# Performance work log

Measured on AMD Instinct MI355X. Metric: run time of the kernel, lower is better.

The kernel has to match this reference:

```python
import jax, jax.numpy as jnp
import numpy as np
import math

B, N, DHID, NH, DHEAD, DFF = 2, 1024, 512, 16, 32, 2048
FACTOR = 0.5 / math.sqrt(DHEAD)


def _ln(x, g, b):
    m = jnp.mean(x, -1, keepdims=True)
    v = jnp.mean((x - m) ** 2, -1, keepdims=True)
    return (x - m) / jnp.sqrt(v + 1e-5) * g + b


def setup_inputs() -> dict:
    key = jax.random.key(0)
    ks = jax.random.split(key, 16)
    rn = lambda k, s, sc=0.02: jax.random.normal(k, s, jnp.float32) * sc
    inp = {}
    inp["H"] = jax.random.normal(ks[0], (B, N, DHID), jnp.float32)
    inp["V"] = jax.random.normal(ks[1], (B, N, 3, DHID), jnp.float32)
    inp["D"] = jax.random.normal(ks[2], (B, N, N), jnp.float32)
    inp["rbf"] = jax.random.normal(ks[3], (B, NH, N, N), jnp.float32)
    inp["mask"] = jnp.ones((B, N), jnp.int32)
    # attention params
    inp["Wq"] = rn(ks[4], (DHID, 4 * DHID)); inp["bq"] = jnp.zeros(4 * DHID)
    inp["Wk"] = rn(ks[5], (DHID, 4 * DHID)); inp["bk"] = jnp.zeros(4 * DHID)
    inp["Wvs"] = rn(ks[6], (DHID, DHID)); inp["bvs"] = jnp.zeros(DHID)
    inp["Wvv"] = rn(ks[7], (DHID, DHID))
    inp["Wo"] = rn(ks[8], (DHID, DHID)); inp["bo"] = jnp.zeros(DHID)
    inp["Wvo"] = rn(ks[9], (DHID, DHID))
    inp["ln1_g"] = jnp.ones(DHID); inp["ln1_b"] = jnp.zeros(DHID)
    # GVP FFN params
    inp["Wlv"] = rn(ks[10], (DHID, 2 * DHID))
    inp["W1"] = rn(ks[11], (2 * DHID, DFF)); inp["b1"] = jnp.zeros(DFF)
    inp["W2"] = rn(ks[12], (DFF, 2 * DHID)); inp["b2"] = jnp.zeros(2 * DHID)
    inp["ln2_g"] = jnp.ones(DHID); inp["ln2_b"] = jnp.zeros(DHID)
    return inp


def reference(H, V, D, rbf, mask, Wq, bq, Wk, bk, Wvs, bvs, Wvv, Wo, bo, Wvo,
              ln1_g, ln1_b, Wlv, W1, b1, W2, b2, ln2_g, ln2_b):
    # ---- self-attention sublayer (pre-LN on H only, residual on H and V) ----
    Hn = _ln(H, ln1_g, ln1_b)
    Hq = (Hn @ Wq + bq).reshape(B, N, NH, 4 * DHEAD)
    Hk = (Hn @ Wk + bk).reshape(B, N, NH, 4 * DHEAD)
    Hv = (Hn @ Wvs + bvs).reshape(B, N, NH, DHEAD)
    # vector values: (B,N,3,DHID) -> (B,N,3,NH,DHEAD) -> (B,N,NH,3,DHEAD) -> (B,N,NH,3*DHEAD)
    Vv = (V @ Wvv).reshape(B, N, 3, NH, DHEAD).transpose(0, 1, 3, 2, 4).reshape(B, N, NH, 3 * DHEAD)
    V_attn = jnp.concatenate([Hv, Vv], axis=-1)  # (B,N,NH,4*DHEAD)
    bias = rbf + D[:, None]  # (B,NH,N,N)
    bias = jnp.where((mask[:, None, None, :] == 0), -jnp.inf, bias)
    scores = jnp.einsum('bnhd,bmhd->bhnm', Hq, Hk) * FACTOR + bias
    attn = jax.nn.softmax(scores, axis=-1)
    res = jnp.einsum('bhnm,bmhd->bnhd', attn, V_attn)  # (B,N,NH,4*DHEAD)
    H_res = res[..., :DHEAD].reshape(B, N, DHID)
    V_res = res[..., DHEAD:].reshape(B, N, NH, 3, DHEAD).transpose(0, 1, 3, 2, 4).reshape(B, N, 3, DHID)
    H = H + (H_res @ Wo + bo)
    V = V + (V_res @ Wvo)
    # ---- GVP FFN sublayer (pre-LN on H only, residual) ----
    Hn = _ln(H, ln2_g, ln2_b)
    Vp = V @ Wlv  # (B,N,3, 2*DHID)
    V1, V2 = Vp[..., :DHID], Vp[..., DHID:]
    scaler = jnp.concatenate([Hn, jnp.linalg.norm(V1, axis=-2)], axis=-1)  # (B,N,2*DHID)
    s = jax.nn.silu(scaler @ W1 + b1) @ W2 + b2  # (B,N,2*DHID)
    H_out, V_upd = s[..., :DHID], s[..., DHID:]
    H = H + H_out
    V = V + V_upd[:, :, None, :] * V2  # vector_act='none'
    return (H, V)
```

## Files before the change

kernel.cpp:

```cpp
#include <hip/hip_runtime.h>
#include <math.h>

constexpr int Bc = 2, Nseq = 1024, Dh = 512, Nh = 16, Dhead = 32;
constexpr float FACT = 0.08838834764831845f;
constexpr float LOG2E = 1.4426950408889634f;

typedef __attribute__((ext_vector_type(8))) __bf16 bf16x8;
typedef __attribute__((ext_vector_type(4))) float f32x4;

__device__ __forceinline__ short f2b(float x) {
    union { float f; unsigned u; } v; v.f = x;
    unsigned r = v.u + 0x7fffu + ((v.u >> 16) & 1u);
    return (short)(r >> 16);
}
__device__ __forceinline__ float b2f(short s) {
    union { unsigned u; float f; } v; v.u = ((unsigned)(unsigned short)s) << 16;
    return v.f;
}

#define GL2LDS(g, s) __builtin_amdgcn_global_load_lds(                  \
    (const void __attribute__((address_space(1)))*)(g),                 \
    (void __attribute__((address_space(3)))*)(s), 16, 0, 0)

__device__ __forceinline__ void mfma_loop(const short* __restrict__ A, int lda,
                                          const short* __restrict__ B, int ldb,
                                          int K, short* __restrict__ smA,
                                          short* __restrict__ smB, f32x4 acc[4][4]) {
    const int tid = threadIdx.x;
    const int lane = tid & 63;
    const int w = tid >> 6;
    const int wr = (w >> 1) * 64, wc = (w & 1) * 64;
    const int lr = lane & 15;
    const int srow = tid >> 3;
    const int scol = tid & 7;
    for (int k0 = 0; k0 < K; k0 += 64) {
        __syncthreads();
#pragma unroll
        for (int r = 0; r < 4; r++) {
            int row = r * 32 + srow;
            int gc = scol ^ (row & 7);
            GL2LDS(A + (long)row * lda + k0 + gc * 8, smA + row * 64 + scol * 8);
            GL2LDS(B + (long)row * ldb + k0 + gc * 8, smB + row * 64 + scol * 8);
        }
        __syncthreads();
#pragma unroll
        for (int h = 0; h < 2; h++) {
            int cb = h * 4 + (lane >> 4);
            bf16x8 af[4], bv[4];
#pragma unroll
            for (int i = 0; i < 4; i++) {
                int row = wr + i * 16 + lr;
                af[i] = *(const bf16x8*)(smA + row * 64 + ((cb ^ (row & 7)) << 3));
            }
#pragma unroll
            for (int j = 0; j < 4; j++) {
                int row = wc + j * 16 + lr;
                bv[j] = *(const bf16x8*)(smB + row * 64 + ((cb ^ (row & 7)) << 3));
            }
            __builtin_amdgcn_s_setprio(1);
#pragma unroll
            for (int i = 0; i < 4; i++)
#pragma unroll
                for (int j = 0; j < 4; j++)
                    acc[i][j] = __builtin_amdgcn_mfma_f32_16x16x32_bf16(af[i], bv[j], acc[i][j], 0, 0, 0);
            __builtin_amdgcn_s_setprio(0);
        }
    }
}

__global__ __launch_bounds__(256) void gemm_bf16(
    const short* __restrict__ A, int lda, long sAz,
    const short* __restrict__ B, int ldb, long sBz,
    void* __restrict__ C, int ldc, long sCz,
    const float* __restrict__ bias,
    const float* __restrict__ resid, int ldr, long sRz,
    short* __restrict__ aux,
    int K, int flags)
{
    __shared__ short smA[128 * 64], smB[128 * 64];
    const long z = blockIdx.z;
    const short* Ab = A + z * sAz + (long)blockIdx.y * 128 * lda;
    const short* Bb = B + z * sBz + (long)blockIdx.x * 128 * ldb;
    f32x4 acc[4][4] = {};
    mfma_loop(Ab, lda, Bb, ldb, K, smA, smB, acc);
    const int tid = threadIdx.x, lane = tid & 63, w = tid >> 6;
    const int wr = (w >> 1) * 64, wc = (w & 1) * 64, lr = lane & 15, r0 = (lane >> 4) * 4;
    const int m0 = blockIdx.y * 128, n0 = blockIdx.x * 128;
    float* Cf = (float*)C; short* Cs = (short*)C;
    const float* rz = resid ? resid + z * sRz : nullptr;
#pragma unroll
    for (int i = 0; i < 4; i++)
#pragma unroll
        for (int j = 0; j < 4; j++) {
            int col = n0 + wc + j * 16 + lr;
            float bv = bias ? bias[col] : 0.f;
#pragma unroll
            for (int q = 0; q < 4; q++) {
                int row = m0 + wr + i * 16 + r0 + q;
                float c = acc[i][j][q] + bv;
                if (rz) c += rz[(long)row * ldr + col];
                if (flags & 1) c = c / (1.f + __expf(-c));
                long off = z * sCz + (long)row * ldc + col;
                if (flags & 2) Cs[off] = f2b(c); else Cf[off] = c;
                if (aux) aux[off] = f2b(c);
            }
        }
}

__global__ __launch_bounds__(256) void gemm_qkv_vvv(
    const short* __restrict__ Hn, const short* __restrict__ WqkvT,
    const short* __restrict__ Vbf, const short* __restrict__ WvvT,
    short* __restrict__ Hqkv, short* __restrict__ VvR,
    const float* __restrict__ bqkv)
{
    __shared__ short smA[128 * 64], smB[128 * 64];
    const bool qkv = blockIdx.y < 16;
    if (!qkv && blockIdx.x >= 4) return;
    const int yy = qkv ? blockIdx.y : blockIdx.y - 16;
    const short* Ab = (qkv ? Hn : Vbf) + (long)yy * 128 * 512;
    const short* Bb = (qkv ? WqkvT : WvvT) + (long)blockIdx.x * 128 * 512;
    f32x4 acc[4][4] = {};
    mfma_loop(Ab, 512, Bb, 512, 512, smA, smB, acc);
    const int tid = threadIdx.x, lane = tid & 63, w = tid >> 6;
    const int wr = (w >> 1) * 64, wc = (w & 1) * 64, lr = lane & 15, r0 = (lane >> 4) * 4;
    const int m0 = yy * 128, n0 = blockIdx.x * 128;
    short* Cs = qkv ? Hqkv : VvR;
    const int ldc = qkv ? 4608 : 512;
#pragma unroll
    for (int i = 0; i < 4; i++)
#pragma unroll
        for (int j = 0; j < 4; j++) {
            int col = n0 + wc + j * 16 + lr;
            float bv = qkv ? bqkv[col] : 0.f;
#pragma unroll
            for (int q = 0; q < 4; q++) {
                int row = m0 + wr + i * 16 + r0 + q;
                Cs[(long)row * ldc + col] = f2b(acc[i][j][q] + bv);
            }
        }
}

__global__ __launch_bounds__(256) void gemm_out(
    const short* __restrict__ Ares, const short* __restrict__ WoT,
    const short* __restrict__ WvoT, float* __restrict__ outHV,
    const float* __restrict__ H, const float* __restrict__ V,
    short* __restrict__ Vbf2, const float* __restrict__ bo)
{
    __shared__ short smA[128 * 64], smB[128 * 64];
    const bool isH = blockIdx.y < 16;
    const short* Ab = Ares + (long)blockIdx.y * 128 * 512;
    const short* Bb = (isH ? WoT : WvoT) + (long)blockIdx.x * 128 * 512;
    f32x4 acc[4][4] = {};
    mfma_loop(Ab, 512, Bb, 512, 512, smA, smB, acc);
    const int tid = threadIdx.x, lane = tid & 63, w = tid >> 6;
    const int wr = (w >> 1) * 64, wc = (w & 1) * 64, lr = lane & 15, r0 = (lane >> 4) * 4;
    const int m0 = blockIdx.y * 128, n0 = blockIdx.x * 128;
#pragma unroll
    for (int i = 0; i < 4; i++)
#pragma unroll
        for (int j = 0; j < 4; j++) {
            int col = n0 + wc + j * 16 + lr;
            float bv = isH ? bo[col] : 0.f;
#pragma unroll
            for (int q = 0; q < 4; q++) {
                int row = m0 + wr + i * 16 + r0 + q;
                float c = acc[i][j][q] + bv;
                if (isH) c += H[(long)row * 512 + col];
                else     c += V[(long)(row - 2048) * 512 + col];
                outHV[(long)row * 512 + col] = c;
                if (!isH) Vbf2[(long)(row - 2048) * 512 + col] = f2b(c);
            }
        }
}

__global__ __launch_bounds__(256, 2) void flash_attn(
    const short* __restrict__ Hq, const short* __restrict__ Hk,
    const short* __restrict__ VaT, const float* __restrict__ rbf,
    const float* __restrict__ Dm, const float* __restrict__ maskadd,
    short* __restrict__ Hres, short* __restrict__ Vres, int ldq)
{
    __shared__ short smK[128 * 128];
    __shared__ short smP[4][16 * 128];
    const int xcd = blockIdx.x & 7, idx = blockIdx.x >> 3;
    const int s = (idx >> 4) * 8 + xcd;
    const int qt = idx & 15;
    const int b = s >> 4, h = s & 15;
    const int q0 = qt * 64;
    const int tid = threadIdx.x, lane = tid & 63, w = tid >> 6;
    const int lr = lane & 15, hi = lane >> 4, r0 = hi * 4;
    const int c16 = tid & 15, rS = tid >> 4;
    short* smPw = smP[w];

    bf16x8 qf[4];
    {
        const short* qb = Hq + ((long)b * Nseq + q0 + w * 16 + lr) * ldq + h * 128 + hi * 8;
#pragma unroll
        for (int kk = 0; kk < 4; kk++) qf[kk] = *(const bf16x8*)(qb + kk * 32);
    }

    f32x4 oac[8] = {};
    float ml[4], ll[4];
#pragma unroll
    for (int q = 0; q < 4; q++) { ml[q] = -INFINITY; ll[q] = 0.f; }

    const short* Kg = Hk + (long)b * Nseq * ldq + h * 128;
    const short* Vg = VaT + (long)s * 128 * Nseq;
    const float* rbb = rbf + ((long)s * Nseq + q0 + w * 16) * Nseq;
    const float* Dbb = Dm + ((long)b * Nseq + q0 + w * 16) * Nseq;
    const float* mab = maskadd + b * Nseq;
    const int bcol = (lane & 31) * 4, brow2 = lane >> 5;
    const int bch = bcol >> 3;

    for (int kt = 0; kt < 8; kt++) {
        __syncthreads();
#pragma unroll
        for (int r = 0; r < 8; r++) {
            int row = rS + r * 16;
            int gc = c16 ^ (row & 15);
            GL2LDS(Kg + (long)(kt * 128 + row) * ldq + gc * 8, smK + row * 128 + c16 * 8);
        }
        {
            short4 hb[8];
            float4 mk = *(const float4*)(mab + kt * 128 + bcol);
#pragma unroll
            for (int it = 0; it < 8; it++) {
                int row = it * 2 + brow2;
                float4 rv = *(const float4*)(rbb + (long)row * Nseq + kt * 128 + bcol);
                float4 dv = *(const float4*)(Dbb + (long)row * Nseq + kt * 128 + bcol);
                hb[it].x = f2b((rv.x + dv.x + mk.x) * LOG2E);
                hb[it].y = f2b((rv.y + dv.y + mk.y) * LOG2E);
                hb[it].z = f2b((rv.z + dv.z + mk.z) * LOG2E);
                hb[it].w = f2b((rv.w + dv.w + mk.w) * LOG2E);
            }
#pragma unroll
            for (int it = 0; it < 8; it++) {
                int row = it * 2 + brow2;
                *(short4*)(&smPw[row * 128 + ((bch ^ (row & 7)) << 3) + (bcol & 7)]) = hb[it];
            }
        }
        __syncthreads();

        f32x4 sac[8] = {};
#pragma unroll
        for (int kk = 0; kk < 4; kk++) {
            int cb = kk * 4 + hi;
            bf16x8 kv8[8];
#pragma unroll
            for (int j = 0; j < 8; j++) {
                int row = j * 16 + lr;
                kv8[j] = *(const bf16x8*)(smK + row * 128 + ((cb ^ (row & 15)) << 3));
            }
            __builtin_amdgcn_s_setprio(1);
#pragma unroll
            for (int j = 0; j < 8; j++)
                sac[j] = __builtin_amdgcn_mfma_f32_16x16x32_bf16(qf[kk], kv8[j], sac[j], 0, 0, 0);
            __builtin_amdgcn_s_setprio(0);
        }
        float tmax[4];
#pragma unroll
        for (int q = 0; q < 4; q++) tmax[q] = -INFINITY;
#pragma unroll
        for (int j = 0; j < 8; j++) {
            int col = j * 16 + lr;
            int ch = col >> 3, in8 = col & 7;
#pragma unroll
            for (int q = 0; q < 4; q++) {
                int row = r0 + q;
                float x = sac[j][q] + b2f(smPw[row * 128 + ((ch ^ (row & 7)) << 3) + in8]);
                sac[j][q] = x;
                tmax[q] = fmaxf(tmax[q], x);
            }
        }
#pragma unroll
        for (int st = 1; st < 16; st <<= 1)
#pragma unroll
            for (int q = 0; q < 4; q++) tmax[q] = fmaxf(tmax[q], __shfl_xor(tmax[q], st));
        float dm = -INFINITY;
#pragma unroll
        for (int q = 0; q < 4; q++) dm = fmaxf(dm, tmax[q] - ml[q]);
        if (!__all(dm <= 8.f)) {
#pragma unroll
            for (int q = 0; q < 4; q++) {
                float mn = fmaxf(ml[q], tmax[q]);
                float sc = exp2f(ml[q] - mn);
                ml[q] = mn;
                ll[q] *= sc;
#pragma unroll
                for (int j = 0; j < 8; j++) oac[j][q] *= sc;
            }
        }
        float rsum[4] = {0.f, 0.f, 0.f, 0.f};
#pragma unroll
        for (int j = 0; j < 8; j++) {
            int col = j * 16 + lr;
            int ch = col >> 3, in8 = col & 7;
#pragma unroll
            for (int q = 0; q < 4; q++) {
                float p = exp2f(sac[j][q] - ml[q]);
                rsum[q] += p;
                int row = r0 + q;
                smPw[row * 128 + ((ch ^ (row & 7)) << 3) + in8] = f2b(p);
            }
        }
#pragma unroll
        for (int st = 1; st < 16; st <<= 1)
#pragma unroll
            for (int q = 0; q < 4; q++) rsum[q] += __shfl_xor(rsum[q], st);
#pragma unroll
        for (int q = 0; q < 4; q++) ll[q] += rsum[q];
#pragma unroll
        for (int kk = 0; kk < 4; kk++) {
            int cb = kk * 4 + hi;
            bf16x8 paf = *(const bf16x8*)(&smPw[lr * 128 + ((cb ^ (lr & 7)) << 3)]);
            bf16x8 vv[8];
#pragma unroll
            for (int j = 0; j < 8; j++)
                vv[j] = *(const bf16x8*)(Vg + (long)(j * 16 + lr) * Nseq + kt * 128 + cb * 8);
            __builtin_amdgcn_s_setprio(1);
#pragma unroll
            for (int j = 0; j < 8; j++)
                oac[j] = __builtin_amdgcn_mfma_f32_16x16x32_bf16(paf, vv[j], oac[j], 0, 0, 0);
            __builtin_amdgcn_s_setprio(0);
        }
    }
    float inv[4];
#pragma unroll
    for (int q = 0; q < 4; q++) inv[q] = 1.f / ll[q];
#pragma unroll
    for (int j = 0; j < 8; j++) {
        int d = j * 16 + lr;
#pragma unroll
        for (int q = 0; q < 4; q++) {
            int n = q0 + w * 16 + r0 + q;
            float o = oac[j][q] * inv[q];
            if (d < 32) Hres[((long)b * Nseq + n) * 512 + h * 32 + d] = f2b(o);
            else {
                int c3 = (d - 32) >> 5, dd = (d - 32) & 31;
                Vres[(((long)b * Nseq + n) * 3 + c3) * 512 + h * 32 + dd] = f2b(o);
            }
        }
    }
}

struct PrepJobs {
    const float* W[9];
    short* Wt[9];
    int K[9], N[9], nx[9], base[9];
    float scale[9];
    int base_convk, base_bprep, base_mask;
    const float* V; short* Vbf;
    const float* bq; const float* bk; const float* bvs; float* bqkv;
    const int* mask; float* maskadd;
};

__global__ __launch_bounds__(256) void prep_k(PrepJobs a) {
    int bid = blockIdx.x;
    int tid = threadIdx.x;
    if (bid >= a.base_convk) {
        if (bid < a.base_bprep) {
            int i = (bid - a.base_convk) * 256 + tid;
            float4 v = ((const float4*)a.V)[i];
            short4 s;
            s.x = f2b(v.x); s.y = f2b(v.y); s.z = f2b(v.z); s.w = f2b(v.w);
            ((short4*)a.Vbf)[i] = s;
        } else if (bid < a.base_mask) {
            int i = (bid - a.base_bprep) * 256 + tid;
            float v;
            if (i < 2048) v = a.bq[i] * (FACT * LOG2E);
            else if (i < 4096) v = a.bk[i - 2048];
            else v = a.bvs[i - 4096];
            a.bqkv[i] = v;
        } else {
            int i = (bid - a.base_mask) * 256 + tid;
            a.maskadd[i] = a.mask[i] ? 0.f : -1e30f;
        }
        return;
    }
    int j = 0;
#pragma unroll
    for (int t = 1; t < 9; t++) j = (bid >= a.base[t]) ? t : j;
    const float* W = a.W[j];
    short* Wt = a.Wt[j];
    int K = a.K[j], N = a.N[j];
    float scale = a.scale[j];
    int local = bid - a.base[j];
    int nx = a.nx[j];
    int bx = local % nx, by = local / nx;
    __shared__ float t[32][33];
    int n0 = bx * 32, k0 = by * 32;
    int tx = tid & 31, ty = tid >> 5;
#pragma unroll
    for (int r = 0; r < 4; r++) t[ty + r * 8][tx] = W[(long)(k0 + ty + r * 8) * N + n0 + tx];
    __syncthreads();
#pragma unroll
    for (int r = 0; r < 4; r++) Wt[(long)(n0 + ty + r * 8) * K + k0 + tx] = f2b(t[tx][ty + r * 8] * scale);
}

__device__ __forceinline__ void stv(float* p, float v) { *p = v; }
__device__ __forceinline__ void stv(short* p, float v) { *p = f2b(v); }

template <typename OT>
__global__ __launch_bounds__(256) void ln_kernel(const float* __restrict__ x,
                                                 const float* __restrict__ g,
                                                 const float* __restrict__ b,
                                                 OT* __restrict__ y, int ldo) {
    int row = blockIdx.x;
    const float* xr = x + (long)row * Dh;
    OT* yr = y + (long)row * ldo;
    int tid = threadIdx.x;
    float v0 = xr[tid], v1 = xr[tid + 256];
    __shared__ float red[256];
    red[tid] = v0 + v1;
    __syncthreads();
    for (int o = 128; o > 0; o >>= 1) { if (tid < o) red[tid] += red[tid + o]; __syncthreads(); }
    float mean = red[0] * (1.0f / Dh);
    __syncthreads();
    float d0 = v0 - mean, d1 = v1 - mean;
    red[tid] = d0 * d0 + d1 * d1;
    __syncthreads();
    for (int o = 128; o > 0; o >>= 1) { if (tid < o) red[tid] += red[tid + o]; __syncthreads(); }
    float rstd = rsqrtf(red[0] * (1.0f / Dh) + 1e-5f);
    stv(&yr[tid], d0 * rstd * g[tid] + b[tid]);
    stv(&yr[tid + 256], d1 * rstd * g[tid + 256] + b[tid + 256]);
}

__global__ __launch_bounds__(256) void vattn_t(const short* __restrict__ Hv, int ldh,
                                               const short* __restrict__ Vv,
                                               short* __restrict__ VaT) {
    int idx = blockIdx.x * 256 + threadIdx.x;
    int m = idx & 1023, d = (idx >> 10) & 127;
    int s = idx >> 17; int b = s >> 4, h = s & 15;
    short val;
    if (d < 32) val = Hv[((long)b * Nseq + m) * ldh + h * 32 + d];
    else {
        int c3 = (d - 32) >> 5, dd = (d - 32) & 31;
        val = Vv[(((long)b * Nseq + m) * 3 + c3) * 512 + h * 32 + dd];
    }
    VaT[idx] = val;
}

__global__ __launch_bounds__(256) void scaler_norm(const float* __restrict__ Vp,
                                                   short* __restrict__ scaler) {
    int idx = blockIdx.x * 256 + threadIdx.x;
    int jj = (idx & 127) * 4;
    int row = idx >> 7;
    float4 ss = {0.f, 0.f, 0.f, 0.f};
#pragma unroll
    for (int c = 0; c < 3; c++) {
        float4 v = *(const float4*)(Vp + ((long)row * 3 + c) * 1024 + jj);
        ss.x += v.x * v.x; ss.y += v.y * v.y; ss.z += v.z * v.z; ss.w += v.w * v.w;
    }
    short4 o;
    o.x = f2b(sqrtf(ss.x)); o.y = f2b(sqrtf(ss.y));
    o.z = f2b(sqrtf(ss.z)); o.w = f2b(sqrtf(ss.w));
    *(short4*)(scaler + (long)row * 1024 + 512 + jj) = o;
}

__global__ __launch_bounds__(256) void final_k(float* __restrict__ outH,
                                               float* __restrict__ outV,
                                               const float* __restrict__ s,
                                               const float* __restrict__ Vp) {
    int idx = blockIdx.x * 256 + threadIdx.x;
    int jj = (idx & 127) * 4;
    int row = idx >> 7;
    float4 s1 = *(const float4*)(s + (long)row * 1024 + jj);
    float4 h = *(const float4*)(outH + (long)row * 512 + jj);
    h.x += s1.x; h.y += s1.y; h.z += s1.z; h.w += s1.w;
    *(float4*)(outH + (long)row * 512 + jj) = h;
    float4 vu = *(const float4*)(s + (long)row * 1024 + 512 + jj);
#pragma unroll
    for (int c = 0; c < 3; c++) {
        float4 v2 = *(const float4*)(Vp + ((long)row * 3 + c) * 1024 + 512 + jj);
        float* vp = outV + ((long)row * 3 + c) * 512 + jj;
        float4 vo = *(const float4*)vp;
        vo.x += vu.x * v2.x; vo.y += vu.y * v2.y;
        vo.z += vu.z * v2.z; vo.w += vu.w * v2.w;
        *(float4*)vp = vo;
    }
}

extern "C" void kernel_launch(void* const* d_in, const int* in_sizes, int n_in,
                              void* d_out, int out_size, void* d_ws, size_t ws_size,
                              hipStream_t stream) {
    const float* H    = (const float*)d_in[0];
    const float* V    = (const float*)d_in[1];
    const float* Dm   = (const float*)d_in[2];
    const float* rbf  = (const float*)d_in[3];
    const int*   mask = (const int*)d_in[4];
    const float* Wq   = (const float*)d_in[5];
    const float* bq   = (const float*)d_in[6];
    const float* Wk   = (const float*)d_in[7];
    const float* bk   = (const float*)d_in[8];
    const float* Wvs  = (const float*)d_in[9];
    const float* bvs  = (const float*)d_in[10];
    const float* Wvv  = (const float*)d_in[11];
    const float* Wo   = (const float*)d_in[12];
    const float* bo   = (const float*)d_in[13];
    const float* Wvo  = (const float*)d_in[14];
    const float* ln1g = (const float*)d_in[15];
    const float* ln1b = (const float*)d_in[16];
    const float* Wlv  = (const float*)d_in[17];
    const float* W1   = (const float*)d_in[18];
    const float* b1   = (const float*)d_in[19];
    const float* W2   = (const float*)d_in[20];
    const float* b2   = (const float*)d_in[21];
    const float* ln2g = (const float*)d_in[22];
    const float* ln2b = (const float*)d_in[23];

    char* wsb = (char*)d_ws;
    auto KB = [&](long kb) { return (void*)(wsb + kb * 1024l); };
    short* WqkvT = (short*)KB(0);
    short* WvvT  = (short*)KB(4608);
    short* WoT   = (short*)KB(5120);
    short* WvoT  = (short*)KB(5632);
    short* WlvT  = (short*)KB(6144);
    short* W1T   = (short*)KB(7168);
    short* W2T   = (short*)KB(11264);
    float* bqkv  = (float*)KB(15360);
    short* Hqkv = (short*)KB(15384);
    short* VvR  = (short*)KB(33816);
    short* VaT  = (short*)KB(39960);
    short* Hn   = (short*)KB(48152);
    short* Vbf  = (short*)KB(50200);
    short* Hres = (short*)KB(56344);
    short* Vres = (short*)KB(58392);
    float* maskadd = (float*)KB(64536);
    short* Vbf2   = (short*)KB(15384);
    float* Vp     = (float*)KB(21528);
    short* scaler = (short*)KB(46104);
    short* t1     = (short*)KB(50200);
    float* sbuf   = (float*)KB(58392);

    float* outH = (float*)d_out;
    float* outV = outH + (size_t)Bc * Nseq * Dh;

    PrepJobs a;
    const float* srcs[9] = {Wq, Wk, Wvs, Wvv, Wo, Wvo, Wlv, W1, W2};
    short* dsts[9] = {WqkvT, WqkvT + 2048 * 512, WqkvT + 4096 * 512,
                      WvvT, WoT, WvoT, WlvT, W1T, W2T};
    int Ks[9] = {512, 512, 512, 512, 512, 512, 512, 1024, 2048};
    int Ns[9] = {2048, 2048, 512, 512, 512, 512, 1024, 2048, 1024};
    float scl[9] = {FACT * LOG2E, 1.f, 1.f, 1.f, 1.f, 1.f, 1.f, 1.f, 1.f};
    int base = 0;
    for (int j = 0; j < 9; j++) {
        a.W[j] = srcs[j]; a.Wt[j] = dsts[j];
        a.K[j] = Ks[j]; a.N[j] = Ns[j];
        a.nx[j] = Ns[j] / 32;
        a.scale[j] = scl[j];
        a.base[j] = base;
        base += (Ns[j] / 32) * (Ks[j] / 32);
    }
    a.base_convk = base;
    a.base_bprep = base + 3072;
    a.base_mask  = base + 3072 + 18;
    a.V = V; a.Vbf = Vbf;
    a.bq = bq; a.bk = bk; a.bvs = bvs; a.bqkv = bqkv;
    a.mask = mask; a.maskadd = maskadd;
    int prep_blocks = a.base_mask + 8;
    prep_k<<<prep_blocks, 256, 0, stream>>>(a);

    ln_kernel<short><<<2048, 256, 0, stream>>>(H, ln1g, ln1b, Hn, 512);
    gemm_qkv_vvv<<<dim3(36, 64), 256, 0, stream>>>(Hn, WqkvT, Vbf, WvvT, Hqkv, VvR, bqkv);
    vattn_t<<<16384, 256, 0, stream>>>(Hqkv + 4096, 4608, VvR, VaT);

    flash_attn<<<dim3(512), 256, 0, stream>>>(Hqkv, Hqkv + 2048, VaT, rbf, Dm, maskadd,
                                              Hres, Vres, 4608);

    gemm_out<<<dim3(4, 64), 256, 0, stream>>>(Hres, WoT, WvoT, outH, H, V, Vbf2, bo);
    ln_kernel<short><<<2048, 256, 0, stream>>>(outH, ln2g, ln2b, scaler, 1024);
    gemm_bf16<<<dim3(8, 48, 1), 256, 0, stream>>>(Vbf2, 512, 0, WlvT, 512, 0, Vp, 1024, 0,
                                                  nullptr, nullptr, 0, 0, nullptr, 512, 0);
    scaler_norm<<<1024, 256, 0, stream>>>(Vp, scaler);
    gemm_bf16<<<dim3(16, 16, 1), 256, 0, stream>>>(scaler, 1024, 0, W1T, 1024, 0, t1, 2048, 0,
                                                   b1, nullptr, 0, 0, nullptr, 1024, 3);
    gemm_bf16<<<dim3(8, 16, 1), 256, 0, stream>>>(t1, 2048, 0, W2T, 2048, 0, sbuf, 1024, 0,
                                                  b2, nullptr, 0, 0, nullptr, 2048, 0);
    final_k<<<1024, 256, 0, stream>>>(outH, outV, sbuf, Vp);
}
```

Measured before the change: 305.8 us.

## Stage V tiles in LDS for flash attention and vectorize V transpose

The flash attention kernel now copies both K and V tiles into swizzled shared memory through registers, replacing the direct global_load_lds path for K and the per-wave global reads of V. All four waves share each V tile instead of each fetching it from global memory. The softmax exponentials are computed and summed before the P writes to LDS, and the s_setprio hints are removed. The VaT transpose kernel now reads 8 bf16 values per thread with one vector load instead of one scalar per thread, while its stores stay scalar. Shared memory per block doubles, which may limit the two-blocks-per-CU occupancy, and the register-staged copy adds VGPR pressure.

```diff
diff --git a/kernel.cpp b/kernel.cpp
--- a/kernel.cpp
+++ b/kernel.cpp
@@ -180,7 +180,8 @@
     short* __restrict__ Hres, short* __restrict__ Vres, int ldq)
 {
     __shared__ short smK[128 * 128];
-    __shared__ short smP[4][16 * 128];
+    __shared__ short smV[128 * 128];
+    __shared__ short smP[4 * 16 * 128];
     const int xcd = blockIdx.x & 7, idx = blockIdx.x >> 3;
     const int s = (idx >> 4) * 8 + xcd;
     const int qt = idx & 15;
@@ -189,7 +190,7 @@
     const int tid = threadIdx.x, lane = tid & 63, w = tid >> 6;
     const int lr = lane & 15, hi = lane >> 4, r0 = hi * 4;
     const int c16 = tid & 15, rS = tid >> 4;
-    short* smPw = smP[w];
+    short* smPw = smP + w * 2048;
 
     bf16x8 qf[4];
     {
@@ -209,15 +210,27 @@
     const float* Dbb = Dm + ((long)b * Nseq + q0 + w * 16) * Nseq;
     const float* mab = maskadd + b * Nseq;
     const int bcol = (lane & 31) * 4, brow2 = lane >> 5;
-    const int bch = bcol >> 3;
 
     for (int kt = 0; kt < 8; kt++) {
         __syncthreads();
-#pragma unroll
-        for (int r = 0; r < 8; r++) {
-            int row = rS + r * 16;
-            int gc = c16 ^ (row & 15);
-            GL2LDS(Kg + (long)(kt * 128 + row) * ldq + gc * 8, smK + row * 128 + c16 * 8);
+        {
+            bf16x8 t8[8];
+#pragma unroll
+            for (int r = 0; r < 8; r++)
+                t8[r] = *(const bf16x8*)(Kg + (long)(kt * 128 + rS + r * 16) * ldq + c16 * 8);
+#pragma unroll
+            for (int r = 0; r < 8; r++) {
+                int row = rS + r * 16;
+                *(bf16x8*)(smK + row * 128 + (c16 ^ (row & 15)) * 8) = t8[r];
+            }
+#pragma unroll
+            for (int r = 0; r < 8; r++)
+                t8[r] = *(const bf16x8*)(Vg + (long)(rS + r * 16) * Nseq + kt * 128 + c16 * 8);
+#pragma unroll
+            for (int r = 0; r < 8; r++) {
+                int row = rS + r * 16;
+                *(bf16x8*)(smV + row * 128 + (c16 ^ (row & 15)) * 8) = t8[r];
+            }
         }
         {
             short4 hb[8];
@@ -232,10 +245,11 @@
                 hb[it].z = f2b((rv.z + dv.z + mk.z) * LOG2E);
                 hb[it].w = f2b((rv.w + dv.w + mk.w) * LOG2E);
             }
+            int ch = bcol >> 3;
 #pragma unroll
             for (int it = 0; it < 8; it++) {
                 int row = it * 2 + brow2;
-                *(short4*)(&smPw[row * 128 + ((bch ^ (row & 7)) << 3) + (bcol & 7)]) = hb[it];
+                *(short4*)(smPw + row * 128 + ((ch ^ (row & 7)) << 3) + (bcol & 7)) = hb[it];
             }
         }
         __syncthreads();
@@ -250,11 +264,9 @@
                 int row = j * 16 + lr;
                 kv8[j] = *(const bf16x8*)(smK + row * 128 + ((cb ^ (row & 15)) << 3));
             }
-            __builtin_amdgcn_s_setprio(1);
 #pragma unroll
             for (int j = 0; j < 8; j++)
                 sac[j] = __builtin_amdgcn_mfma_f32_16x16x32_bf16(qf[kk], kv8[j], sac[j], 0, 0, 0);
-            __builtin_amdgcn_s_setprio(0);
         }
         float tmax[4];
 #pragma unroll
@@ -291,36 +303,42 @@
         }
         float rsum[4] = {0.f, 0.f, 0.f, 0.f};
 #pragma unroll
+        for (int j = 0; j < 8; j++)
+#pragma unroll
+            for (int q = 0; q < 4; q++) {
+                float p = exp2f(sac[j][q] - ml[q]);
+                sac[j][q] = p;
+                rsum[q] += p;
+            }
+#pragma unroll
+        for (int st = 1; st < 16; st <<= 1)
+#pragma unroll
+            for (int q = 0; q < 4; q++) rsum[q] += __shfl_xor(rsum[q], st);
+#pragma unroll
+        for (int q = 0; q < 4; q++) ll[q] += rsum[q];
+#pragma unroll
         for (int j = 0; j < 8; j++) {
             int col = j * 16 + lr;
             int ch = col >> 3, in8 = col & 7;
 #pragma unroll
             for (int q = 0; q < 4; q++) {
-                float p = exp2f(sac[j][q] - ml[q]);
-                rsum[q] += p;
                 int row = r0 + q;
-                smPw[row * 128 + ((ch ^ (row & 7)) << 3) + in8] = f2b(p);
-            }
-        }
-#pragma unroll
-        for (int st = 1; st < 16; st <<= 1)
-#pragma unroll
-            for (int q = 0; q < 4; q++) rsum[q] += __shfl_xor(rsum[q], st);
-#pragma unroll
-        for (int q = 0; q < 4; q++) ll[q] += rsum[q];
+                smPw[row * 128 + ((ch ^ (row & 7)) << 3) + in8] = f2b(sac[j][q]);
+            }
+        }
 #pragma unroll
         for (int kk = 0; kk < 4; kk++) {
             int cb = kk * 4 + hi;
-            bf16x8 paf = *(const bf16x8*)(&smPw[lr * 128 + ((cb ^ (lr & 7)) << 3)]);
+            bf16x8 paf = *(const bf16x8*)(smPw + lr * 128 + ((cb ^ (lr & 7)) << 3));
             bf16x8 vv[8];
 #pragma unroll
-            for (int j = 0; j < 8; j++)
-                vv[j] = *(const bf16x8*)(Vg + (long)(j * 16 + lr) * Nseq + kt * 128 + cb * 8);
-            __builtin_amdgcn_s_setprio(1);
+            for (int j = 0; j < 8; j++) {
+                int row = j * 16 + lr;
+                vv[j] = *(const bf16x8*)(smV + row * 128 + ((cb ^ (row & 15)) << 3));
+            }
 #pragma unroll
             for (int j = 0; j < 8; j++)
                 oac[j] = __builtin_amdgcn_mfma_f32_16x16x32_bf16(paf, vv[j], oac[j], 0, 0, 0);
-            __builtin_amdgcn_s_setprio(0);
         }
     }
     float inv[4];
@@ -424,19 +442,25 @@
     stv(&yr[tid + 256], d1 * rstd * g[tid + 256] + b[tid + 256]);
 }
 
-__global__ __launch_bounds__(256) void vattn_t(const short* __restrict__ Hv, int ldh,
-                                               const short* __restrict__ Vv,
-                                               short* __restrict__ VaT) {
+__global__ __launch_bounds__(256) void vattn_t8(const short* __restrict__ Hv, int ldh,
+                                                const short* __restrict__ Vv,
+                                                short* __restrict__ VaT) {
     int idx = blockIdx.x * 256 + threadIdx.x;
-    int m = idx & 1023, d = (idx >> 10) & 127;
-    int s = idx >> 17; int b = s >> 4, h = s & 15;
-    short val;
-    if (d < 32) val = Hv[((long)b * Nseq + m) * ldh + h * 32 + d];
-    else {
-        int c3 = (d - 32) >> 5, dd = (d - 32) & 31;
-        val = Vv[(((long)b * Nseq + m) * 3 + c3) * 512 + h * 32 + dd];
-    }
-    VaT[idx] = val;
+    int m = idx & 1023;
+    int c = (idx >> 10) & 15;
+    int s = idx >> 14;
+    int b = s >> 4, h = s & 15;
+    bf16x8 v;
+    if (c < 4) {
+        v = *(const bf16x8*)(Hv + ((long)b * Nseq + m) * ldh + h * 32 + c * 8);
+    } else {
+        int c3 = (c - 4) >> 2, dd = ((c - 4) & 3) * 8;
+        v = *(const bf16x8*)(Vv + (((long)b * Nseq + m) * 3 + c3) * 512 + h * 32 + dd);
+    }
+    short* out = VaT + (long)s * 128 * 1024 + (long)c * 8 * 1024 + m;
+    const short* vs = (const short*)&v;
+#pragma unroll
+    for (int e = 0; e < 8; e++) out[e * 1024] = vs[e];
 }
 
 __global__ __launch_bounds__(256) void scaler_norm(const float* __restrict__ Vp,
@@ -561,7 +585,7 @@
 
     ln_kernel<short><<<2048, 256, 0, stream>>>(H, ln1g, ln1b, Hn, 512);
     gemm_qkv_vvv<<<dim3(36, 64), 256, 0, stream>>>(Hn, WqkvT, Vbf, WvvT, Hqkv, VvR, bqkv);
-    vattn_t<<<16384, 256, 0, stream>>>(Hqkv + 4096, 4608, VvR, VaT);
+    vattn_t8<<<2048, 256, 0, stream>>>(Hqkv + 4096, 4608, VvR, VaT);
 
     flash_attn<<<dim3(512), 256, 0, stream>>>(Hqkv, Hqkv + 2048, VaT, rbf, Dm, maskadd,
                                               Hres, Vres, 4608);
```

Measured after the change: 255.6 us. 16.4% less time.
